# Performance work log

Hardware: AMD Instinct MI355X
Metric: run time of the kernel (lower is better)

The kernel has to match this reference:

```python
import jax, jax.numpy as jnp
import numpy as np

N_NODES = 50000
N_EDGES = 1600000
IN_FEAT = 256
OUT_FEAT = 64


def setup_inputs() -> dict:
    key = jax.random.key(0)
    k1, k2, k3, k4, k5, k6 = jax.random.split(key, 6)
    feat = jax.random.normal(k1, (N_NODES, IN_FEAT), dtype=jnp.float32)
    edge_src = jax.random.randint(k2, (N_EDGES,), 0, N_NODES, dtype=jnp.int32)
    edge_dst = jax.random.randint(k3, (N_EDGES,), 0, N_NODES, dtype=jnp.int32)
    edge_weight = jax.random.uniform(k4, (N_EDGES,), dtype=jnp.float32)
    # Xavier-uniform init as in reset_parameters
    bound = float(np.sqrt(6.0 / (IN_FEAT + OUT_FEAT)))
    W_self = jax.random.uniform(k5, (IN_FEAT, OUT_FEAT), minval=-bound, maxval=bound, dtype=jnp.float32)
    W_neigh = jax.random.uniform(k6, (IN_FEAT, OUT_FEAT), minval=-bound, maxval=bound, dtype=jnp.float32)
    return {"feat": feat, "edge_src": edge_src, "edge_dst": edge_dst,
            "edge_weight": edge_weight, "W_self": W_self, "W_neigh": W_neigh}


def reference(feat, edge_src, edge_dst, edge_weight, W_self, W_neigh):
    # neigh_feat = spmm(adj, feat): row dst aggregates weighted neighbors src
    gathered = feat[edge_src] * edge_weight[:, None]          # [E, in_feat]
    neigh_feat = jax.ops.segment_sum(gathered, edge_dst, num_segments=N_NODES)  # [N, in_feat]
    self_feat = feat @ W_self                                 # [N, out_feat]
    neigh_feat = neigh_feat @ W_neigh                         # [N, out_feat]
    out = jax.nn.relu(self_feat + neigh_feat)
    # dropout p=0.0 -> identity
    return out
```

## Files before the change

### kernel.cpp

```cpp
#include <hip/hip_runtime.h>

#define IN_FEAT 256
#define OUT_FEAT 64
#define BBITS 5
#define BSZ 32
#define NBMAX 1568
#define CAPB 1280
#define CNT_STRIDE 16
#define EPB 4096
#define SCT 512

typedef __attribute__((ext_vector_type(8))) short bf16x8;
typedef __attribute__((ext_vector_type(4))) float f32x4;

static __device__ __forceinline__ short f2bf(float f) {
    unsigned u = __float_as_uint(f);
    unsigned r = (u + 0x7FFFu + ((u >> 16) & 1u)) >> 16;
    return (short)r;
}
static __device__ __forceinline__ float bflo(unsigned v) {
    return __uint_as_float(v << 16);
}
static __device__ __forceinline__ float bfhi(unsigned v) {
    return __uint_as_float(v & 0xFFFF0000u);
}

__global__ __launch_bounds__(256) void prep(
    const float* __restrict__ Wself,
    const float* __restrict__ Wneigh,
    bf16x8* __restrict__ Wfrag,
    int* __restrict__ cnt, int cnt_words)
{
    const int t = blockIdx.x * 256 + threadIdx.x;
    if (t < 4096) {
        const int kstep = t >> 9;
        const int ntile = (t >> 6) & 7;
        const int lane  = t & 63;
        const int quad  = lane >> 4;
        const int n     = ntile * 16 + (lane & 15);
        const float* src = (n < OUT_FEAT) ? (Wself + n) : (Wneigh + (n - OUT_FEAT));
        const int k0 = kstep * 32 + quad * 8;
        bf16x8 v;
#pragma unroll
        for (int j = 0; j < 8; ++j) v[j] = f2bf(src[(size_t)(k0 + j) * OUT_FEAT]);
        Wfrag[t] = v;
    }
    const int nthr = gridDim.x * 256;
    for (int i = t; i < cnt_words; i += nthr) cnt[i] = 0;
}

__global__ __launch_bounds__(512) void gemm_scatter(
    const float* __restrict__ feat,
    const bf16x8* __restrict__ Wfrag,
    unsigned short* __restrict__ accSelf,
    unsigned short* __restrict__ Pn,
    const int* __restrict__ esrc,
    const int* __restrict__ edst,
    const float* __restrict__ ew,
    int* __restrict__ cnt,
    unsigned* __restrict__ binned,
    int n_nodes, int n_edges, int NB)
{
    __shared__ int hist[NBMAX];
    __shared__ int cur[NBMAX];

    const int t    = threadIdx.x;
    const int wave = t >> 6;
    const int lane = t & 63;

    for (int i = t; i < NB; i += SCT) hist[i] = 0;

    {
        const int row0 = (blockIdx.x * 8 + wave) * 16;
        if (row0 < n_nodes) {
            const int quad = lane >> 4;
            const int l15  = lane & 15;

            f32x4 c[8];
#pragma unroll
            for (int i = 0; i < 8; ++i) c[i] = (f32x4){0.f, 0.f, 0.f, 0.f};

            const int arow = min(row0 + l15, n_nodes - 1);
            const float* afeat = feat + (size_t)arow * IN_FEAT + quad * 8;

#pragma unroll
            for (int kstep = 0; kstep < 8; ++kstep) {
                const float4 x = *(const float4*)(afeat + kstep * 32);
                const float4 y = *(const float4*)(afeat + kstep * 32 + 4);
                bf16x8 a;
                a[0] = f2bf(x.x); a[1] = f2bf(x.y); a[2] = f2bf(x.z); a[3] = f2bf(x.w);
                a[4] = f2bf(y.x); a[5] = f2bf(y.y); a[6] = f2bf(y.z); a[7] = f2bf(y.w);
                bf16x8 b[8];
#pragma unroll
                for (int nt = 0; nt < 8; ++nt) b[nt] = Wfrag[(kstep * 8 + nt) * 64 + lane];
#pragma unroll
                for (int nt = 0; nt < 8; ++nt)
                    c[nt] = __builtin_amdgcn_mfma_f32_16x16x32_bf16(a, b[nt], c[nt], 0, 0, 0);
            }

#pragma unroll
            for (int nt = 0; nt < 8; ++nt) {
                unsigned short* dst = (nt < 4) ? accSelf : Pn;
                const int col = (nt & 3) * 16 + l15;
#pragma unroll
                for (int r = 0; r < 4; ++r) {
                    const int row = row0 + quad * 4 + r;
                    if (row < n_nodes)
                        dst[(size_t)row * OUT_FEAT + col] = (unsigned short)f2bf(c[nt][r]);
                }
            }
        }
    }
    __syncthreads();

    const long base = (long)blockIdx.x * EPB;
#pragma unroll
    for (int k = 0; k < 8; ++k) {
        const long idx = base + k * SCT + t;
        if (idx < n_edges) atomicAdd(&hist[edst[idx] >> BBITS], 1);
    }
    __syncthreads();

    for (int i = t; i < NB; i += SCT) {
        const int h = hist[i];
        cur[i] = h ? atomicAdd(&cnt[(size_t)i * CNT_STRIDE], h) : 0;
    }
    __syncthreads();

#pragma unroll
    for (int k = 0; k < 8; ++k) {
        const long idx = base + k * SCT + t;
        if (idx < n_edges) {
            const int d = edst[idx];
            const unsigned s  = (unsigned)esrc[idx];
            const unsigned wq = (unsigned)__float2int_rn(ew[idx] * 2047.0f);
            const unsigned rec = ((unsigned)(d & (BSZ - 1)) << 27) | (wq << 16) | s;
            const int b = d >> BBITS;
            const int slot = atomicAdd(&cur[b], 1);
            if (slot < CAPB) binned[(size_t)b * CAPB + slot] = rec;
        }
    }
}

__global__ __launch_bounds__(256) void bucket_gather(
    const unsigned* __restrict__ binned,
    const int* __restrict__ cnt,
    const unsigned short* __restrict__ Pn,
    const unsigned short* __restrict__ accSelf,
    float* __restrict__ out, int n_nodes, int NB)
{
    __shared__ unsigned raw[CAPB];
    __shared__ int2 sepk[CAPB];
    __shared__ int  hcnt[BSZ];
    __shared__ int  hoff[BSZ + 1];
    __shared__ int  hcur[BSZ];
    __shared__ int  snrec;

    const int b = blockIdx.x;
    const int t = threadIdx.x;

    if (t == 0) snrec = min(cnt[(size_t)b * CNT_STRIDE], CAPB);
    if (t < BSZ) hcnt[t] = 0;
    __syncthreads();
    const int nrec  = snrec;
    const int nrec4 = (nrec + 3) >> 2;

    {
        const uint4* rb4 = (const uint4*)(binned + (size_t)b * CAPB);
        uint4* rw4 = (uint4*)raw;
        for (int i = t; i < nrec4; i += 256) {
            const uint4 v = rb4[i];
            rw4[i] = v;
            const int e0 = i * 4;
            if (e0 + 0 < nrec) atomicAdd(&hcnt[v.x >> 27], 1);
            if (e0 + 1 < nrec) atomicAdd(&hcnt[v.y >> 27], 1);
            if (e0 + 2 < nrec) atomicAdd(&hcnt[v.z >> 27], 1);
            if (e0 + 3 < nrec) atomicAdd(&hcnt[v.w >> 27], 1);
        }
    }
    __syncthreads();
    if (t == 0) {
        int run = 0;
#pragma unroll
        for (int k = 0; k < BSZ; ++k) { hoff[k] = run; run += hcnt[k]; }
        hoff[BSZ] = run;
    }
    __syncthreads();
    if (t < BSZ) hcur[t] = hoff[t];
    __syncthreads();

    for (int i = t; i < nrec; i += 256) {
        const unsigned p = raw[i];
        const int pos = atomicAdd(&hcur[p >> 27], 1);
        const float w = (float)((p >> 16) & 0x7FFu) * (1.0f / 2047.0f);
        sepk[pos] = make_int2((int)(p & 0xFFFFu), __float_as_int(w));
    }
    __syncthreads();

    const int wv   = t >> 6;
    const int lane = t & 63;
    const int half = lane >> 5;
    const int c2   = (lane & 31) * 2;

#pragma unroll
    for (int ldn = wv * 8; ldn < wv * 8 + 8; ++ldn) {
        const int dst = b * BSZ + ldn;
        if (dst >= n_nodes) break;
        const int beg = hoff[ldn];
        const int end = hoff[ldn + 1];

        float A0[8], A1[8];
#pragma unroll
        for (int j = 0; j < 8; ++j) { A0[j] = 0.f; A1[j] = 0.f; }

        int e = beg + half;
        for (; e + 14 < end; e += 16) {
#pragma unroll
            for (int j = 0; j < 8; ++j) {
                const int2 p = sepk[e + 2 * j];
                const unsigned v = *(const unsigned*)(Pn + (size_t)p.x * OUT_FEAT + c2);
                const float w = __int_as_float(p.y);
                A0[j] += w * bflo(v);
                A1[j] += w * bfhi(v);
            }
        }
        for (; e + 6 < end; e += 8) {
#pragma unroll
            for (int j = 0; j < 4; ++j) {
                const int2 p = sepk[e + 2 * j];
                const unsigned v = *(const unsigned*)(Pn + (size_t)p.x * OUT_FEAT + c2);
                const float w = __int_as_float(p.y);
                A0[j] += w * bflo(v);
                A1[j] += w * bfhi(v);
            }
        }
        for (; e < end; e += 2) {
            const int2 p = sepk[e];
            const unsigned v = *(const unsigned*)(Pn + (size_t)p.x * OUT_FEAT + c2);
            const float w = __int_as_float(p.y);
            A0[0] += w * bflo(v);
            A1[0] += w * bfhi(v);
        }
        float s0 = ((A0[0] + A0[1]) + (A0[2] + A0[3])) + ((A0[4] + A0[5]) + (A0[6] + A0[7]));
        float s1 = ((A1[0] + A1[1]) + (A1[2] + A1[3])) + ((A1[4] + A1[5]) + (A1[6] + A1[7]));
        s0 += __shfl_xor(s0, 32, 64);
        s1 += __shfl_xor(s1, 32, 64);
        if (half == 0) {
            const unsigned sv = *(const unsigned*)(accSelf + (size_t)dst * OUT_FEAT + c2);
            float2 o;
            o.x = fmaxf(bflo(sv) + s0, 0.f);
            o.y = fmaxf(bfhi(sv) + s1, 0.f);
            *(float2*)(out + (size_t)dst * OUT_FEAT + c2) = o;
        }
    }
}

extern "C" void kernel_launch(void* const* d_in, const int* in_sizes, int n_in,
                              void* d_out, int out_size, void* d_ws, size_t ws_size,
                              hipStream_t stream) {
    const float* feat   = (const float*)d_in[0];
    const int*   esrc   = (const int*)  d_in[1];
    const int*   edst   = (const int*)  d_in[2];
    const float* ew     = (const float*)d_in[3];
    const float* Wself  = (const float*)d_in[4];
    const float* Wneigh = (const float*)d_in[5];

    const int n_nodes = in_sizes[0] / IN_FEAT;
    const int n_edges = in_sizes[1];
    const int NB = (n_nodes + BSZ - 1) / BSZ;

    bf16x8* Wfrag           = (bf16x8*)d_ws;
    unsigned short* accSelf = (unsigned short*)((char*)d_ws + 65536);
    unsigned short* Pn      = accSelf + (size_t)n_nodes * OUT_FEAT;
    unsigned* binned = (unsigned*)(Pn + (size_t)n_nodes * OUT_FEAT);
    int*   cnt     = (int*)(binned + (size_t)NB * CAPB);
    float* out     = (float*)d_out;

    const int cnt_words = NB * CNT_STRIDE;
    prep<<<64, 256, 0, stream>>>(Wself, Wneigh, Wfrag, cnt, cnt_words);

    const int sblocks = (n_edges + EPB - 1) / EPB;
    const int tblocks = (((n_nodes + 15) / 16) + 7) / 8;
    const int fblocks = (sblocks > tblocks) ? sblocks : tblocks;
    gemm_scatter<<<fblocks, SCT, 0, stream>>>(
        feat, Wfrag, accSelf, Pn, esrc, edst, ew, cnt, binned, n_nodes, n_edges, NB);

    bucket_gather<<<NB, 256, 0, stream>>>(binned, cnt, Pn, accSelf, out, n_nodes, NB);
}
```

Measured before the change: 202.6 us.

## Coarsen edge buckets to 128 nodes and locally sort edges before scattering

Edges are now binned into 391 buckets of 128 destination nodes instead of 1563 buckets of 32. Each scatter block first counting-sorts its 4096 edges in shared memory, so writes to the global bucket arrays come out contiguous rather than scattered. Records become 8-byte int2 pairs holding the full float weight instead of an 11-bit quantised weight, which doubles the binned traffic but restores weight accuracy. The gather kernel uses 512 threads per bucket with a parallel scan in place of a serial prefix. Each block now needs more shared memory, which may lower occupancy.

```diff
diff --git a/kernel.cpp b/kernel.cpp
--- a/kernel.cpp
+++ b/kernel.cpp
@@ -2,10 +2,10 @@
 
 #define IN_FEAT 256
 #define OUT_FEAT 64
-#define BBITS 5
-#define BSZ 32
-#define NBMAX 1568
-#define CAPB 1280
+#define BBITS2 7
+#define GSZ 128
+#define NB2 391
+#define CAPB 5120
 #define CNT_STRIDE 16
 #define EPB 4096
 #define SCT 512
@@ -49,7 +49,7 @@
     for (int i = t; i < cnt_words; i += nthr) cnt[i] = 0;
 }
 
-__global__ __launch_bounds__(512) void gemm_scatter(
+__global__ __launch_bounds__(SCT) void gemm_scatter(
     const float* __restrict__ feat,
     const bf16x8* __restrict__ Wfrag,
     unsigned short* __restrict__ accSelf,
@@ -58,17 +58,21 @@
     const int* __restrict__ edst,
     const float* __restrict__ ew,
     int* __restrict__ cnt,
-    unsigned* __restrict__ binned,
-    int n_nodes, int n_edges, int NB)
+    int2* __restrict__ binned,
+    int n_nodes, int n_edges)
 {
-    __shared__ int hist[NBMAX];
-    __shared__ int cur[NBMAX];
+    __shared__ int  hist[NB2];
+    __shared__ int  scan[SCT];
+    __shared__ int  loff[NB2];
+    __shared__ int  lcur[NB2];
+    __shared__ int  gbase[NB2];
+    __shared__ int2 sorted[EPB];
 
     const int t    = threadIdx.x;
     const int wave = t >> 6;
     const int lane = t & 63;
 
-    for (int i = t; i < NB; i += SCT) hist[i] = 0;
+    for (int i = t; i < NB2; i += SCT) hist[i] = 0;
 
     {
         const int row0 = (blockIdx.x * 8 + wave) * 16;
@@ -114,86 +118,102 @@
     __syncthreads();
 
     const long base = (long)blockIdx.x * EPB;
+    int2 rec[8];
+    int  bin[8];
+    bool ok[8];
 #pragma unroll
     for (int k = 0; k < 8; ++k) {
         const long idx = base + k * SCT + t;
-        if (idx < n_edges) atomicAdd(&hist[edst[idx] >> BBITS], 1);
-    }
-    __syncthreads();
-
-    for (int i = t; i < NB; i += SCT) {
-        const int h = hist[i];
-        cur[i] = h ? atomicAdd(&cnt[(size_t)i * CNT_STRIDE], h) : 0;
-    }
-    __syncthreads();
-
-#pragma unroll
-    for (int k = 0; k < 8; ++k) {
-        const long idx = base + k * SCT + t;
-        if (idx < n_edges) {
+        ok[k] = idx < n_edges;
+        if (ok[k]) {
             const int d = edst[idx];
-            const unsigned s  = (unsigned)esrc[idx];
-            const unsigned wq = (unsigned)__float2int_rn(ew[idx] * 2047.0f);
-            const unsigned rec = ((unsigned)(d & (BSZ - 1)) << 27) | (wq << 16) | s;
-            const int b = d >> BBITS;
-            const int slot = atomicAdd(&cur[b], 1);
-            if (slot < CAPB) binned[(size_t)b * CAPB + slot] = rec;
-        }
-    }
-}
-
-__global__ __launch_bounds__(256) void bucket_gather(
-    const unsigned* __restrict__ binned,
+            rec[k] = make_int2((d << 16) | esrc[idx], __float_as_int(ew[idx]));
+            bin[k] = d >> BBITS2;
+            atomicAdd(&hist[bin[k]], 1);
+        }
+    }
+    __syncthreads();
+
+    scan[t] = (t < NB2) ? hist[t] : 0;
+    __syncthreads();
+    for (int off = 1; off < SCT; off <<= 1) {
+        const int u = (t >= off) ? scan[t - off] : 0;
+        __syncthreads();
+        scan[t] += u;
+        __syncthreads();
+    }
+    if (t < NB2) {
+        const int h = hist[t];
+        const int lo = scan[t] - h;
+        loff[t] = lo;
+        lcur[t] = lo;
+        gbase[t] = h ? atomicAdd(&cnt[(size_t)t * CNT_STRIDE], h) : 0;
+    }
+    __syncthreads();
+
+#pragma unroll
+    for (int k = 0; k < 8; ++k)
+        if (ok[k]) sorted[atomicAdd(&lcur[bin[k]], 1)] = rec[k];
+    __syncthreads();
+
+    const int tot = (int)min((long)EPB, n_edges - base);
+    for (int i = t; i < tot; i += SCT) {
+        const int2 p = sorted[i];
+        const int b = ((unsigned)p.x >> 16) >> BBITS2;
+        const int ofs = gbase[b] + (i - loff[b]);
+        if (ofs < CAPB) binned[(size_t)b * CAPB + ofs] = p;
+    }
+}
+
+__global__ __launch_bounds__(512) void bucket_gather(
+    const int2* __restrict__ binned,
     const int* __restrict__ cnt,
     const unsigned short* __restrict__ Pn,
     const unsigned short* __restrict__ accSelf,
-    float* __restrict__ out, int n_nodes, int NB)
+    float* __restrict__ out, int n_nodes)
 {
-    __shared__ unsigned raw[CAPB];
     __shared__ int2 sepk[CAPB];
-    __shared__ int  hcnt[BSZ];
-    __shared__ int  hoff[BSZ + 1];
-    __shared__ int  hcur[BSZ];
+    __shared__ int  hcnt[GSZ];
+    __shared__ int  scan2[GSZ];
+    __shared__ int  hoff[GSZ + 1];
+    __shared__ int  hcur[GSZ];
     __shared__ int  snrec;
 
     const int b = blockIdx.x;
     const int t = threadIdx.x;
 
     if (t == 0) snrec = min(cnt[(size_t)b * CNT_STRIDE], CAPB);
-    if (t < BSZ) hcnt[t] = 0;
-    __syncthreads();
-    const int nrec  = snrec;
-    const int nrec4 = (nrec + 3) >> 2;
-
-    {
-        const uint4* rb4 = (const uint4*)(binned + (size_t)b * CAPB);
-        uint4* rw4 = (uint4*)raw;
-        for (int i = t; i < nrec4; i += 256) {
-            const uint4 v = rb4[i];
-            rw4[i] = v;
-            const int e0 = i * 4;
-            if (e0 + 0 < nrec) atomicAdd(&hcnt[v.x >> 27], 1);
-            if (e0 + 1 < nrec) atomicAdd(&hcnt[v.y >> 27], 1);
-            if (e0 + 2 < nrec) atomicAdd(&hcnt[v.z >> 27], 1);
-            if (e0 + 3 < nrec) atomicAdd(&hcnt[v.w >> 27], 1);
-        }
-    }
-    __syncthreads();
-    if (t == 0) {
-        int run = 0;
-#pragma unroll
-        for (int k = 0; k < BSZ; ++k) { hoff[k] = run; run += hcnt[k]; }
-        hoff[BSZ] = run;
-    }
-    __syncthreads();
-    if (t < BSZ) hcur[t] = hoff[t];
-    __syncthreads();
-
-    for (int i = t; i < nrec; i += 256) {
-        const unsigned p = raw[i];
-        const int pos = atomicAdd(&hcur[p >> 27], 1);
-        const float w = (float)((p >> 16) & 0x7FFu) * (1.0f / 2047.0f);
-        sepk[pos] = make_int2((int)(p & 0xFFFFu), __float_as_int(w));
+    if (t < GSZ) hcnt[t] = 0;
+    __syncthreads();
+    const int nrec = snrec;
+    const int2* rb = binned + (size_t)b * CAPB;
+
+    for (int i = t; i < nrec; i += 512)
+        atomicAdd(&hcnt[((unsigned)rb[i].x >> 16) & (GSZ - 1)], 1);
+    __syncthreads();
+
+    if (t < GSZ) scan2[t] = hcnt[t];
+    __syncthreads();
+    for (int off = 1; off < GSZ; off <<= 1) {
+        int u = 0;
+        if (t < GSZ && t >= off) u = scan2[t - off];
+        __syncthreads();
+        if (t < GSZ) scan2[t] += u;
+        __syncthreads();
+    }
+    if (t < GSZ) {
+        const int lo = scan2[t] - hcnt[t];
+        hoff[t] = lo;
+        hcur[t] = lo;
+    }
+    if (t == 0) hoff[GSZ] = nrec;
+    __syncthreads();
+
+    for (int i = t; i < nrec; i += 512) {
+        const int2 p = rb[i];
+        const int dl = ((unsigned)p.x >> 16) & (GSZ - 1);
+        const int pos = atomicAdd(&hcur[dl], 1);
+        sepk[pos] = make_int2(p.x & 0xFFFF, p.y);
     }
     __syncthreads();
 
@@ -203,8 +223,8 @@
     const int c2   = (lane & 31) * 2;
 
 #pragma unroll
-    for (int ldn = wv * 8; ldn < wv * 8 + 8; ++ldn) {
-        const int dst = b * BSZ + ldn;
+    for (int ldn = wv * 16; ldn < wv * 16 + 16; ++ldn) {
+        const int dst = b * GSZ + ldn;
         if (dst >= n_nodes) break;
         const int beg = hoff[ldn];
         const int end = hoff[ldn + 1];
@@ -267,23 +287,22 @@
 
     const int n_nodes = in_sizes[0] / IN_FEAT;
     const int n_edges = in_sizes[1];
-    const int NB = (n_nodes + BSZ - 1) / BSZ;
 
     bf16x8* Wfrag           = (bf16x8*)d_ws;
     unsigned short* accSelf = (unsigned short*)((char*)d_ws + 65536);
     unsigned short* Pn      = accSelf + (size_t)n_nodes * OUT_FEAT;
-    unsigned* binned = (unsigned*)(Pn + (size_t)n_nodes * OUT_FEAT);
-    int*   cnt     = (int*)(binned + (size_t)NB * CAPB);
+    int2*  binned  = (int2*)(Pn + (size_t)n_nodes * OUT_FEAT);
+    int*   cnt     = (int*)(binned + (size_t)NB2 * CAPB);
     float* out     = (float*)d_out;
 
-    const int cnt_words = NB * CNT_STRIDE;
+    const int cnt_words = NB2 * CNT_STRIDE;
     prep<<<64, 256, 0, stream>>>(Wself, Wneigh, Wfrag, cnt, cnt_words);
 
     const int sblocks = (n_edges + EPB - 1) / EPB;
     const int tblocks = (((n_nodes + 15) / 16) + 7) / 8;
     const int fblocks = (sblocks > tblocks) ? sblocks : tblocks;
     gemm_scatter<<<fblocks, SCT, 0, stream>>>(
-        feat, Wfrag, accSelf, Pn, esrc, edst, ew, cnt, binned, n_nodes, n_edges, NB);
-
-    bucket_gather<<<NB, 256, 0, stream>>>(binned, cnt, Pn, accSelf, out, n_nodes, NB);
-}
+        feat, Wfrag, accSelf, Pn, esrc, edst, ew, cnt, binned, n_nodes, n_edges);
+
+    bucket_gather<<<NB2, 512, 0, stream>>>(binned, cnt, Pn, accSelf, out, n_nodes);
+}
```

Measured after the change: 182.7 us. 1.11x faster.
